# Performance work log

Hardware: AMD Instinct MI355X
Metric: run time of the kernel (lower is better)

## Reference

```python
import jax, jax.numpy as jnp
import numpy as np


def setup_inputs() -> dict:
    key = jax.random.key(0)
    ks = jax.random.split(key, 7)
    B, HW, C, H = 32, 3136, 512, 128
    return {
        "c_embed": jax.random.normal(ks[0], (B * HW, C), dtype=jnp.float32),
        "w_embed": jax.random.normal(ks[1], (B * HW, C), dtype=jnp.float32),
        "h_embed": jax.random.normal(ks[2], (B * HW, C), dtype=jnp.float32),
        "fc1_w": jax.random.normal(ks[3], (H, C), dtype=jnp.float32) * 0.05,
        "fc1_b": jax.random.normal(ks[4], (H,), dtype=jnp.float32) * 0.05,
        "fc2_w": jax.random.normal(ks[5], (3 * C, H), dtype=jnp.float32) * 0.05,
        "fc2_b": jax.random.normal(ks[6], (3 * C,), dtype=jnp.float32) * 0.05,
        "B": 32,
    }


def reference(c_embed, w_embed, h_embed, fc1_w, fc1_b, fc2_w, fc2_b, B):
    N, C = c_embed.shape
    HW = N // B
    # (1) global mean over HW of the sum of the three embeddings -> (B, C)
    s = (c_embed + w_embed + h_embed).reshape(B, HW, C).mean(axis=1)
    # (2) 2-layer MLP: fc1 -> GELU(tanh approx, matching gelu_fast) -> fc2
    y1 = jax.nn.gelu(s @ fc1_w.T + fc1_b, approximate=True)          # (B, hidden)
    logits = y1 @ fc2_w.T + fc2_b                                    # (B, 3*C)
    # (3) 3-way softmax: kernel indexes logits[j*C + c] => layout (B, 3, C),
    #     softmax over the 3 branches
    w = jax.nn.softmax(logits.reshape(B, 3, C), axis=1)              # (B, 3, C)
    w0 = jnp.repeat(w[:, 0, :], HW, axis=0)                          # (B*HW, C)
    w1 = jnp.repeat(w[:, 1, :], HW, axis=0)
    w2 = jnp.repeat(w[:, 2, :], HW, axis=0)
    # (4) broadcast weighted sum
    return c_embed * w0 + w_embed * w1 + h_embed * w2
```

## Files before the change

kernel.cpp:

```cpp
#include <hip/hip_runtime.h>

#define B_   32
#define HW_  3136
#define C_   512
#define H_   128

__global__ __launch_bounds__(256) void ps_kernel(
    const float4* __restrict__ c4,
    const float4* __restrict__ w4,
    const float4* __restrict__ h4,
    float4* __restrict__ partial,
    int rows)
{
    const int k    = blockIdx.x;
    const int b    = blockIdx.y;
    const int CH   = gridDim.x;
    const int col4 = threadIdx.x & 127;
    const int rl   = threadIdx.x >> 7;

    long base = ((long)b * HW_ + (long)k * rows + rl) * (C_ / 4) + col4;
    float4 acc = make_float4(0.f, 0.f, 0.f, 0.f);

    #pragma unroll 4
    for (int r = 0; r < rows; r += 2) {
        const float4 a = c4[base];
        const float4 v = w4[base];
        const float4 u = h4[base];
        acc.x += a.x + v.x + u.x;
        acc.y += a.y + v.y + u.y;
        acc.z += a.z + v.z + u.z;
        acc.w += a.w + v.w + u.w;
        base += 2 * (C_ / 4);
    }

    __shared__ float4 red[128];
    if (rl == 1) red[col4] = acc;
    __syncthreads();
    if (rl == 0) {
        const float4 o = red[col4];
        acc.x += o.x; acc.y += o.y; acc.z += o.z; acc.w += o.w;
        partial[((long)b * CH + k) * (C_ / 4) + col4] = acc;
    }
}

__global__ __launch_bounds__(256) void mlp_kernel(
    const float* __restrict__ partial,
    const float* __restrict__ fc1_w,
    const float* __restrict__ fc1_b,
    const float* __restrict__ fc2_w,
    const float* __restrict__ fc2_b,
    float* __restrict__ wbuf,
    int CH)
{
    __shared__ float s_lds[C_];
    __shared__ float y_lds[H_];

    const int b = blockIdx.x;
    const int t = threadIdx.x;

    for (int c = t; c < C_; c += 256) {
        float acc = 0.f;
        const float* __restrict__ p = partial + (long)b * CH * C_ + c;
        for (int k = 0; k < CH; ++k) acc += p[(long)k * C_];
        s_lds[c] = acc * (1.0f / (float)HW_);
    }
    __syncthreads();

    if (t < H_) {
        float acc = fc1_b[t];
        const float* __restrict__ wr = fc1_w + (long)t * C_;
        #pragma unroll 8
        for (int c = 0; c < C_; ++c) acc += s_lds[c] * wr[c];
        const float x = acc;
        const float u = 0.7978845608028654f * (x + 0.044715f * x * x * x);
        y_lds[t] = 0.5f * x * (1.0f + tanhf(u));
    }
    __syncthreads();

    for (int c = t; c < C_; c += 256) {
        float lg[3];
        #pragma unroll
        for (int j = 0; j < 3; ++j) {
            const int row = j * C_ + c;
            float acc = fc2_b[row];
            const float* __restrict__ wr = fc2_w + (long)row * H_;
            #pragma unroll 8
            for (int h = 0; h < H_; ++h) acc += y_lds[h] * wr[h];
            lg[j] = acc;
        }
        const float m  = fmaxf(lg[0], fmaxf(lg[1], lg[2]));
        const float e0 = __expf(lg[0] - m);
        const float e1 = __expf(lg[1] - m);
        const float e2 = __expf(lg[2] - m);
        const float inv = 1.0f / (e0 + e1 + e2);
        float* __restrict__ wb = wbuf + (long)b * 3 * C_;
        wb[0 * C_ + c] = e0 * inv;
        wb[1 * C_ + c] = e1 * inv;
        wb[2 * C_ + c] = e2 * inv;
    }
}

__global__ __launch_bounds__(256) void out_kernel(
    const float4* __restrict__ c4,
    const float4* __restrict__ w4,
    const float4* __restrict__ h4,
    const float4* __restrict__ wb4,
    float4* __restrict__ o4)
{
    const int blk  = blockIdx.x;
    const int b    = blockIdx.y;
    const int t    = threadIdx.x;
    const int col4 = t & 127;

    const float4* __restrict__ wb = wb4 + (long)b * (3 * C_ / 4);
    const float4 w0 = wb[col4];
    const float4 w1 = wb[128 + col4];
    const float4 w2 = wb[256 + col4];

    long idx = (long)b * (HW_ * (C_ / 4)) + (long)blk * 4096 + t;
    #pragma unroll 4
    for (int it = 0; it < 16; ++it) {
        const float4 a = c4[idx];
        const float4 v = w4[idx];
        const float4 u = h4[idx];
        float4 o;
        o.x = a.x * w0.x + v.x * w1.x + u.x * w2.x;
        o.y = a.y * w0.y + v.y * w1.y + u.y * w2.y;
        o.z = a.z * w0.z + v.z * w1.z + u.z * w2.z;
        o.w = a.w * w0.w + v.w * w1.w + u.w * w2.w;
        o4[idx] = o;
        idx += 256;
    }
}

extern "C" void kernel_launch(void* const* d_in, const int* in_sizes, int n_in,
                              void* d_out, int out_size, void* d_ws, size_t ws_size,
                              hipStream_t stream)
{
    const float* c_e   = (const float*)d_in[0];
    const float* w_e   = (const float*)d_in[1];
    const float* h_e   = (const float*)d_in[2];
    const float* fc1_w = (const float*)d_in[3];
    const float* fc1_b = (const float*)d_in[4];
    const float* fc2_w = (const float*)d_in[5];
    const float* fc2_b = (const float*)d_in[6];
    float* out = (float*)d_out;

    int CH = 98;
    {
        const size_t need98 = ((size_t)B_ * 98 * C_ + (size_t)B_ * 3 * C_) * 4;
        const size_t need49 = ((size_t)B_ * 49 * C_ + (size_t)B_ * 3 * C_) * 4;
        if (ws_size < need98) CH = 49;
        if (ws_size < need49) CH = 32;
    }
    const int rows = HW_ / CH;

    float* partial = (float*)d_ws;
    float* wbuf    = partial + (long)B_ * CH * C_;

    ps_kernel<<<dim3(CH, B_), 256, 0, stream>>>(
        (const float4*)c_e, (const float4*)w_e, (const float4*)h_e,
        (float4*)partial, rows);
    mlp_kernel<<<B_, 256, 0, stream>>>(partial, fc1_w, fc1_b, fc2_w, fc2_b, wbuf, CH);
    out_kernel<<<dim3(98, B_), 256, 0, stream>>>(
        (const float4*)c_e, (const float4*)w_e, (const float4*)h_e,
        (const float4*)wbuf, (float4*)out);
}
```

Measured before the change: 390.0 us.

## Fix reduction split at 49 chunks with interleaved prefetch; grid-stride output kernel

The partial-sum kernel now uses a fixed 49 blocks per batch. Each block reads interleaved row pairs with a stride of 49*256 float4s rather than a contiguous row range, and a software prefetch of the next iteration's loads is added. The MLP reduction loop is fully unrolled over the now-constant chunk count. The output kernel becomes a grid-stride loop over 2048 blocks that recomputes the batch index and reloads the three weight vectors each iteration. This adds an integer division per element and drops the workspace-size fallback, which is a risk if the workspace is small.

```diff
diff --git a/kernel.cpp b/kernel.cpp
--- a/kernel.cpp
+++ b/kernel.cpp
@@ -4,34 +4,44 @@
 #define HW_  3136
 #define C_   512
 #define H_   128
+#define CH_  49
+#define BPB_ (HW_ * (C_ / 4))
 
 __global__ __launch_bounds__(256) void ps_kernel(
     const float4* __restrict__ c4,
     const float4* __restrict__ w4,
     const float4* __restrict__ h4,
-    float4* __restrict__ partial,
-    int rows)
+    float4* __restrict__ partial)
 {
-    const int k    = blockIdx.x;
+    const int bx   = blockIdx.x;
     const int b    = blockIdx.y;
-    const int CH   = gridDim.x;
-    const int col4 = threadIdx.x & 127;
-    const int rl   = threadIdx.x >> 7;
+    const int t    = threadIdx.x;
+    const int col4 = t & 127;
+    const int rl   = t >> 7;
 
-    long base = ((long)b * HW_ + (long)k * rows + rl) * (C_ / 4) + col4;
+    const int STRIDE = CH_ * 256;
+    long idx = (long)b * BPB_ + bx * 256 + t;
+
     float4 acc = make_float4(0.f, 0.f, 0.f, 0.f);
 
+    float4 a0 = c4[idx], v0 = w4[idx], u0 = h4[idx];
     #pragma unroll 4
-    for (int r = 0; r < rows; r += 2) {
-        const float4 a = c4[base];
-        const float4 v = w4[base];
-        const float4 u = h4[base];
-        acc.x += a.x + v.x + u.x;
-        acc.y += a.y + v.y + u.y;
-        acc.z += a.z + v.z + u.z;
-        acc.w += a.w + v.w + u.w;
-        base += 2 * (C_ / 4);
+    for (int it = 1; it < 32; ++it) {
+        const long nidx = idx + STRIDE;
+        const float4 a1 = c4[nidx];
+        const float4 v1 = w4[nidx];
+        const float4 u1 = h4[nidx];
+        acc.x += a0.x + v0.x + u0.x;
+        acc.y += a0.y + v0.y + u0.y;
+        acc.z += a0.z + v0.z + u0.z;
+        acc.w += a0.w + v0.w + u0.w;
+        a0 = a1; v0 = v1; u0 = u1;
+        idx = nidx;
     }
+    acc.x += a0.x + v0.x + u0.x;
+    acc.y += a0.y + v0.y + u0.y;
+    acc.z += a0.z + v0.z + u0.z;
+    acc.w += a0.w + v0.w + u0.w;
 
     __shared__ float4 red[128];
     if (rl == 1) red[col4] = acc;
@@ -39,7 +49,7 @@
     if (rl == 0) {
         const float4 o = red[col4];
         acc.x += o.x; acc.y += o.y; acc.z += o.z; acc.w += o.w;
-        partial[((long)b * CH + k) * (C_ / 4) + col4] = acc;
+        partial[((long)b * CH_ + bx) * (C_ / 4) + col4] = acc;
     }
 }
 
@@ -49,8 +59,7 @@
     const float* __restrict__ fc1_b,
     const float* __restrict__ fc2_w,
     const float* __restrict__ fc2_b,
-    float* __restrict__ wbuf,
-    int CH)
+    float* __restrict__ wbuf)
 {
     __shared__ float s_lds[C_];
     __shared__ float y_lds[H_];
@@ -60,8 +69,9 @@
 
     for (int c = t; c < C_; c += 256) {
         float acc = 0.f;
-        const float* __restrict__ p = partial + (long)b * CH * C_ + c;
-        for (int k = 0; k < CH; ++k) acc += p[(long)k * C_];
+        const float* __restrict__ p = partial + (long)b * CH_ * C_ + c;
+        #pragma unroll
+        for (int k = 0; k < CH_; ++k) acc += p[(long)k * C_];
         s_lds[c] = acc * (1.0f / (float)HW_);
     }
     __syncthreads();
@@ -107,19 +117,17 @@
     const float4* __restrict__ wb4,
     float4* __restrict__ o4)
 {
-    const int blk  = blockIdx.x;
-    const int b    = blockIdx.y;
-    const int t    = threadIdx.x;
-    const int col4 = t & 127;
+    const int total  = B_ * HW_ * (C_ / 4);
+    const int stride = gridDim.x * blockDim.x;
+    const int col4   = (blockIdx.x * blockDim.x + threadIdx.x) & 127;
 
-    const float4* __restrict__ wb = wb4 + (long)b * (3 * C_ / 4);
-    const float4 w0 = wb[col4];
-    const float4 w1 = wb[128 + col4];
-    const float4 w2 = wb[256 + col4];
-
-    long idx = (long)b * (HW_ * (C_ / 4)) + (long)blk * 4096 + t;
-    #pragma unroll 4
-    for (int it = 0; it < 16; ++it) {
+    for (int idx = blockIdx.x * blockDim.x + threadIdx.x; idx < total; idx += stride) {
+        const int row = idx >> 7;
+        const int b   = row / HW_;
+        const float4* __restrict__ wb = wb4 + (long)b * (3 * C_ / 4);
+        const float4 w0 = wb[col4];
+        const float4 w1 = wb[128 + col4];
+        const float4 w2 = wb[256 + col4];
         const float4 a = c4[idx];
         const float4 v = w4[idx];
         const float4 u = h4[idx];
@@ -129,7 +137,6 @@
         o.z = a.z * w0.z + v.z * w1.z + u.z * w2.z;
         o.w = a.w * w0.w + v.w * w1.w + u.w * w2.w;
         o4[idx] = o;
-        idx += 256;
     }
 }
 
@@ -146,23 +153,14 @@
     const float* fc2_b = (const float*)d_in[6];
     float* out = (float*)d_out;
 
-    int CH = 98;
-    {
-        const size_t need98 = ((size_t)B_ * 98 * C_ + (size_t)B_ * 3 * C_) * 4;
-        const size_t need49 = ((size_t)B_ * 49 * C_ + (size_t)B_ * 3 * C_) * 4;
-        if (ws_size < need98) CH = 49;
-        if (ws_size < need49) CH = 32;
-    }
-    const int rows = HW_ / CH;
+    float* partial = (float*)d_ws;
+    float* wbuf    = partial + (long)B_ * CH_ * C_;
 
-    float* partial = (float*)d_ws;
-    float* wbuf    = partial + (long)B_ * CH * C_;
-
-    ps_kernel<<<dim3(CH, B_), 256, 0, stream>>>(
+    ps_kernel<<<dim3(CH_, B_), 256, 0, stream>>>(
         (const float4*)c_e, (const float4*)w_e, (const float4*)h_e,
-        (float4*)partial, rows);
-    mlp_kernel<<<B_, 256, 0, stream>>>(partial, fc1_w, fc1_b, fc2_w, fc2_b, wbuf, CH);
-    out_kernel<<<dim3(98, B_), 256, 0, stream>>>(
+        (float4*)partial);
+    mlp_kernel<<<B_, 256, 0, stream>>>(partial, fc1_w, fc1_b, fc2_w, fc2_b, wbuf);
+    out_kernel<<<2048, 256, 0, stream>>>(
         (const float4*)c_e, (const float4*)w_e, (const float4*)h_e,
         (const float4*)wbuf, (float4*)out);
 }
```

Result: faster. 330.4 us (-15.3%).
